# Kernel tuning notes

Hardware: AMD Instinct MI355X
Metric: run time of the kernel (lower is better)

Reference implementation:

```python
import jax, jax.numpy as jnp
import numpy as np

B, L, D, K, V = 128, 50, 64, 1024, 100000


def setup_inputs() -> dict:
    key = jax.random.key(0)
    ks = jax.random.split(key, 10)
    s = 0.05
    return {
        "history_item_ids": jax.random.randint(ks[0], (B, L), 0, V, dtype=jnp.int32),
        "history_item_masks": jax.random.randint(ks[1], (B, L), 0, 2, dtype=jnp.int32),
        "embedding_table": jax.random.normal(ks[2], (V, D), jnp.float32) * s,
        "code_book": jax.random.normal(ks[3], (K, D), jnp.float32) * 0.1,
        "Wq": jax.random.normal(ks[4], (D, D), jnp.float32) * s,
        "bq": jnp.zeros((D,), jnp.float32),
        "Wk": jax.random.normal(ks[5], (D, D), jnp.float32) * s,
        "bk": jnp.zeros((D,), jnp.float32),
        "Wv": jax.random.normal(ks[6], (D, D), jnp.float32) * s,
        "bv": jnp.zeros((D,), jnp.float32),
        "W_enc": jax.random.normal(ks[7], (2 * D, D), jnp.float32) * s,
        "b_enc": jnp.zeros((D,), jnp.float32),
    }


def reference(history_item_ids, history_item_masks, embedding_table, code_book,
              Wq, bq, Wk, bk, Wv, bv, W_enc, b_enc):
    # mask out padded history positions
    mask = (history_item_masks >= 1).astype(jnp.float32)          # [B, L]
    h = embedding_table[history_item_ids] * mask[..., None]       # [B, L, D]

    # self_attn: attention over ALL B*L flattened tokens (cross-batch, as original)
    flat = h.reshape(-1, D)                                       # [B*L, D]
    q = flat @ Wq + bq
    k = flat @ Wk + bk
    v = flat @ Wv + bv
    scores = (q @ k.T) / jnp.sqrt(jnp.float32(D))                 # [B*L, B*L]
    h = (jax.nn.softmax(scores, axis=-1) @ v).reshape(B, L, D)

    denom = mask.sum(axis=1, keepdims=True)                       # [B, 1]
    hist_mean = h.sum(axis=1) / (denom + 1e-9)                    # [B, D]

    # get_quantized: pairwise sq distances + argmin + codebook lookup
    f = h.reshape(-1, D)                                          # [B*L, D]
    d2 = (jnp.sum(f * f, axis=1, keepdims=True)
          + jnp.sum(code_book * code_book, axis=1)
          - 2.0 * f @ code_book.T)                                # [B*L, K]
    idx = jnp.argmin(d2, axis=1)                                  # [B*L]
    vq = code_book[idx].reshape(B, L, D)                          # one_hot @ code_book == gather
    vq_mean = vq.sum(axis=1) / denom                              # [B, D]

    x = jnp.concatenate([vq_mean, hist_mean], axis=-1)            # [B, 2D]
    return x @ W_enc + b_enc                                      # [B, D]
```

## Files before the change

### kernel.cpp

```cpp
#include <hip/hip_runtime.h>

typedef __attribute__((ext_vector_type(8))) short bf16x8_t;
typedef __attribute__((ext_vector_type(4))) float f32x4_t;

#define B_   128
#define L_   50
#define D_   64
#define N_   6400
#define KC   1024
#define STRD 72

static __device__ __forceinline__ unsigned short f2b(float x) {
    union { float f; unsigned int u; } c; c.f = x;
    return (unsigned short)((c.u + 0x7FFFu + ((c.u >> 16) & 1u)) >> 16);
}

__global__ __launch_bounds__(256) void k_qkv(
    const int* __restrict__ ids, const int* __restrict__ masks,
    const float* __restrict__ emb,
    const float* __restrict__ Wq, const float* __restrict__ bq,
    const float* __restrict__ Wk, const float* __restrict__ bk,
    const float* __restrict__ Wv, const float* __restrict__ bv,
    const float* __restrict__ cbf, const float* __restrict__ benc,
    unsigned short* __restrict__ q, unsigned short* __restrict__ k,
    unsigned short* __restrict__ vt,
    float* __restrict__ cn, unsigned short* __restrict__ cbb,
    float* __restrict__ out)
{
    const int tid = threadIdx.x;
    if (blockIdx.x >= 404) {
        for (int i = tid; i < B_ * 64; i += 256) out[i] = benc[i & 63];
        return;
    }
    if (blockIdx.x >= 400) {
        const int c = (blockIdx.x - 400) * 256 + tid;
        float s = 0.f;
        #pragma unroll
        for (int d4 = 0; d4 < 16; ++d4) {
            float4 x = ((const float4*)cbf)[c * 16 + d4];
            s = fmaf(x.x, x.x, s); s = fmaf(x.y, x.y, s);
            s = fmaf(x.z, x.z, s); s = fmaf(x.w, x.w, s);
            ushort4 u;
            u.x = f2b(x.x); u.y = f2b(x.y); u.z = f2b(x.z); u.w = f2b(x.w);
            *(ushort4*)&cbb[c * 64 + d4 * 4] = u;
        }
        cn[c] = s;
        return;
    }

    __shared__ float Ws[3 * 64 * 64];
    __shared__ float hs[16][64];
    const int n0  = blockIdx.x * 16;

    {
        const float4* wq4 = (const float4*)Wq;
        const float4* wk4 = (const float4*)Wk;
        const float4* wv4 = (const float4*)Wv;
        float4* ws4 = (float4*)Ws;
        #pragma unroll
        for (int i = 0; i < 4; ++i) ws4[i*256 + tid]        = wq4[i*256 + tid];
        #pragma unroll
        for (int i = 0; i < 4; ++i) ws4[1024 + i*256 + tid] = wk4[i*256 + tid];
        #pragma unroll
        for (int i = 0; i < 4; ++i) ws4[2048 + i*256 + tid] = wv4[i*256 + tid];
    }
    {
        const int t  = tid >> 4, c4 = tid & 15;
        const int n  = n0 + t;
        const int id = ids[n];
        const float m = (masks[n] >= 1) ? 1.0f : 0.0f;
        float4 e = ((const float4*)emb)[id * 16 + c4];
        ((float4*)&hs[t][0])[c4] = make_float4(e.x*m, e.y*m, e.z*m, e.w*m);
    }
    __syncthreads();

    const int j  = tid & 63;
    const int tg = tid >> 6;
    const float bqj = bq[j], bkj = bk[j], bvj = bv[j];
    #pragma unroll
    for (int p = 0; p < 4; ++p) {
        const int t = p * 4 + tg;
        float aq = bqj, ak = bkj, av = bvj;
        #pragma unroll 8
        for (int d = 0; d < 64; ++d) {
            const float hd = hs[t][d];
            aq = fmaf(hd, Ws[d*64 + j],        aq);
            ak = fmaf(hd, Ws[4096 + d*64 + j], ak);
            av = fmaf(hd, Ws[8192 + d*64 + j], av);
        }
        const int n = n0 + t;
        q[n*64 + j]   = f2b(aq);
        k[n*64 + j]   = f2b(ak);
        vt[j*N_ + n]  = f2b(av);
    }
}

__global__ __launch_bounds__(256, 4) void k_attn(
    const unsigned short* __restrict__ qg, const unsigned short* __restrict__ kg,
    const unsigned short* __restrict__ vtg,
    float* __restrict__ opart, float* __restrict__ lpart)
{
    __shared__ unsigned short Qs[32 * STRD];
    __shared__ unsigned short Ks[64 * STRD];
    __shared__ unsigned short Vts[64 * STRD];
    __shared__ unsigned short Ps[32 * STRD];
    __shared__ float Of[32 * 66];
    __shared__ float lred[2][32];

    const int tid  = threadIdx.x;
    const int qt   = blockIdx.x >> 2;
    const int sp   = blockIdx.x & 3;
    const int q0   = qt * 32;
    const int kvb  = sp * 1600;
    const int lane = tid & 63;
    const int w    = tid >> 6;
    const int m    = w & 1;
    const int s    = w >> 1;
    const int lr   = lane & 15;
    const int lg   = lane >> 4;

    {
        const int row = tid >> 3, ch = tid & 7;
        uint4 t = *(const uint4*)&qg[(q0 + row) * 64 + ch * 8];
        *(uint4*)&Qs[row * STRD + ch * 8] = t;
    }
    __syncthreads();
    const bf16x8_t qa0 = *(const bf16x8_t*)&Qs[(m*16 + lr) * STRD +  0 + lg*8];
    const bf16x8_t qa1 = *(const bf16x8_t*)&Qs[(m*16 + lr) * STRD + 32 + lg*8];

    f32x4_t o0 = {0.f,0.f,0.f,0.f}, o1 = {0.f,0.f,0.f,0.f};
    f32x4_t o2 = {0.f,0.f,0.f,0.f}, o3 = {0.f,0.f,0.f,0.f};
    float ls0 = 0.f, ls1 = 0.f, ls2 = 0.f, ls3 = 0.f;
    const float scale = 0.125f;

    for (int st = 0; st < 25; ++st) {
        __syncthreads();
        const int j0 = kvb + st * 64;
        {
            const int row = tid >> 3, ch = tid & 7;
            uint4 a = *(const uint4*)&kg [(j0 + row)      * 64 + ch*8];
            uint4 b = *(const uint4*)&kg [(j0 + row + 32) * 64 + ch*8];
            uint4 c = *(const uint4*)&vtg[ row       * N_ + j0 + ch*8];
            uint4 d = *(const uint4*)&vtg[(row + 32) * N_ + j0 + ch*8];
            *(uint4*)&Ks [ row      * STRD + ch*8] = a;
            *(uint4*)&Ks [(row+32)  * STRD + ch*8] = b;
            *(uint4*)&Vts[ row      * STRD + ch*8] = c;
            *(uint4*)&Vts[(row+32)  * STRD + ch*8] = d;
        }
        __syncthreads();

        #pragma unroll
        for (int t = 0; t < 2; ++t) {
            const int kcol = s*32 + t*16 + lr;
            bf16x8_t kb0 = *(const bf16x8_t*)&Ks[kcol * STRD +  0 + lg*8];
            bf16x8_t kb1 = *(const bf16x8_t*)&Ks[kcol * STRD + 32 + lg*8];
            f32x4_t acc = {0.f,0.f,0.f,0.f};
            acc = __builtin_amdgcn_mfma_f32_16x16x32_bf16(qa0, kb0, acc, 0, 0, 0);
            acc = __builtin_amdgcn_mfma_f32_16x16x32_bf16(qa1, kb1, acc, 0, 0, 0);
            const float p0 = __expf(acc[0] * scale);
            const float p1 = __expf(acc[1] * scale);
            const float p2 = __expf(acc[2] * scale);
            const float p3 = __expf(acc[3] * scale);
            ls0 += p0; ls1 += p1; ls2 += p2; ls3 += p3;
            const int rb = (m*16 + lg*4) * STRD + kcol;
            Ps[rb           ] = f2b(p0);
            Ps[rb +   STRD  ] = f2b(p1);
            Ps[rb + 2*STRD  ] = f2b(p2);
            Ps[rb + 3*STRD  ] = f2b(p3);
        }

        const bf16x8_t pa = *(const bf16x8_t*)&Ps[(m*16 + lr) * STRD + s*32 + lg*8];
        {
            bf16x8_t vb;
            vb = *(const bf16x8_t*)&Vts[( 0 + lr) * STRD + s*32 + lg*8];
            o0 = __builtin_amdgcn_mfma_f32_16x16x32_bf16(pa, vb, o0, 0, 0, 0);
            vb = *(const bf16x8_t*)&Vts[(16 + lr) * STRD + s*32 + lg*8];
            o1 = __builtin_amdgcn_mfma_f32_16x16x32_bf16(pa, vb, o1, 0, 0, 0);
            vb = *(const bf16x8_t*)&Vts[(32 + lr) * STRD + s*32 + lg*8];
            o2 = __builtin_amdgcn_mfma_f32_16x16x32_bf16(pa, vb, o2, 0, 0, 0);
            vb = *(const bf16x8_t*)&Vts[(48 + lr) * STRD + s*32 + lg*8];
            o3 = __builtin_amdgcn_mfma_f32_16x16x32_bf16(pa, vb, o3, 0, 0, 0);
        }
    }

    #pragma unroll
    for (int off = 1; off <= 8; off <<= 1) {
        ls0 += __shfl_xor(ls0, off);
        ls1 += __shfl_xor(ls1, off);
        ls2 += __shfl_xor(ls2, off);
        ls3 += __shfl_xor(ls3, off);
    }
    if (lr == 0) {
        const int rb = m*16 + lg*4;
        lred[s][rb    ] = ls0;
        lred[s][rb + 1] = ls1;
        lred[s][rb + 2] = ls2;
        lred[s][rb + 3] = ls3;
    }

    if (s == 0) {
        #pragma unroll
        for (int r = 0; r < 4; ++r) {
            const int row = m*16 + lg*4 + r;
            Of[row*66 +  0 + lr] = o0[r];
            Of[row*66 + 16 + lr] = o1[r];
            Of[row*66 + 32 + lr] = o2[r];
            Of[row*66 + 48 + lr] = o3[r];
        }
    }
    __syncthreads();
    if (s == 1) {
        float* op = opart + ((size_t)sp * N_ + q0) * 64;
        #pragma unroll
        for (int r = 0; r < 4; ++r) {
            const int row = m*16 + lg*4 + r;
            op[row*64 +  0 + lr] = Of[row*66 +  0 + lr] + o0[r];
            op[row*64 + 16 + lr] = Of[row*66 + 16 + lr] + o1[r];
            op[row*64 + 32 + lr] = Of[row*66 + 32 + lr] + o2[r];
            op[row*64 + 48 + lr] = Of[row*66 + 48 + lr] + o3[r];
        }
    }
    if (tid < 32) lpart[sp*N_ + q0 + tid] = lred[0][tid] + lred[1][tid];
}

__global__ __launch_bounds__(64) void k_vq(
    const float* __restrict__ opart, const float* __restrict__ lpart,
    const unsigned short* __restrict__ cbb, const float* __restrict__ cn,
    const float* __restrict__ cbf, const int* __restrict__ masks,
    const float* __restrict__ Wenc, float* __restrict__ out)
{
    const int lane = threadIdx.x;
    const int n0   = blockIdx.x * 16;
    const int lr   = lane & 15, lg = lane >> 4;
    const int row  = n0 + lr;

    const float l = lpart[row] + lpart[N_ + row] + lpart[2*N_ + row] + lpart[3*N_ + row];
    const float inv = 1.0f / l;

    float fr[16];
    #pragma unroll
    for (int h = 0; h < 2; ++h) {
        const int base = row*64 + h*32 + lg*8;
        float4 s0 = *(const float4*)&opart[base];
        float4 s1 = *(const float4*)&opart[(size_t)N_*64   + base];
        float4 s2 = *(const float4*)&opart[(size_t)N_*64*2 + base];
        float4 s3 = *(const float4*)&opart[(size_t)N_*64*3 + base];
        float4 t0 = *(const float4*)&opart[base + 4];
        float4 t1 = *(const float4*)&opart[(size_t)N_*64   + base + 4];
        float4 t2 = *(const float4*)&opart[(size_t)N_*64*2 + base + 4];
        float4 t3 = *(const float4*)&opart[(size_t)N_*64*3 + base + 4];
        fr[h*8+0] = ((s0.x+s1.x)+s2.x)+s3.x;  fr[h*8+1] = ((s0.y+s1.y)+s2.y)+s3.y;
        fr[h*8+2] = ((s0.z+s1.z)+s2.z)+s3.z;  fr[h*8+3] = ((s0.w+s1.w)+s2.w)+s3.w;
        fr[h*8+4] = ((t0.x+t1.x)+t2.x)+t3.x;  fr[h*8+5] = ((t0.y+t1.y)+t2.y)+t3.y;
        fr[h*8+6] = ((t0.z+t1.z)+t2.z)+t3.z;  fr[h*8+7] = ((t0.w+t1.w)+t2.w)+t3.w;
    }
    bf16x8_t fa0, fa1;
    #pragma unroll
    for (int i = 0; i < 8; ++i) {
        fa0[i] = (short)f2b(fr[i]     * inv);
        fa1[i] = (short)f2b(fr[8 + i] * inv);
    }

    float best0 = 3.0e38f, best1 = 3.0e38f, best2 = 3.0e38f, best3 = 3.0e38f;
    int   bi0 = 0, bi1 = 0, bi2 = 0, bi3 = 0;

    #pragma unroll 4
    for (int st = 0; st < 64; ++st) {
        const int crow = st * 16 + lr;
        bf16x8_t cb0 = *(const bf16x8_t*)&cbb[crow * 64 +  0 + lg*8];
        bf16x8_t cb1 = *(const bf16x8_t*)&cbb[crow * 64 + 32 + lg*8];
        const float cnv = cn[crow];
        f32x4_t acc = {0.f,0.f,0.f,0.f};
        acc = __builtin_amdgcn_mfma_f32_16x16x32_bf16(fa0, cb0, acc, 0, 0, 0);
        acc = __builtin_amdgcn_mfma_f32_16x16x32_bf16(fa1, cb1, acc, 0, 0, 0);
        const float d0 = fmaf(-2.f, acc[0], cnv);
        const float d1 = fmaf(-2.f, acc[1], cnv);
        const float d2 = fmaf(-2.f, acc[2], cnv);
        const float d3 = fmaf(-2.f, acc[3], cnv);
        if (d0 < best0) { best0 = d0; bi0 = crow; }
        if (d1 < best1) { best1 = d1; bi1 = crow; }
        if (d2 < best2) { best2 = d2; bi2 = crow; }
        if (d3 < best3) { best3 = d3; bi3 = crow; }
    }

    #pragma unroll
    for (int off = 1; off <= 8; off <<= 1) {
        float ov; int oi;
        ov = __shfl_xor(best0, off); oi = __shfl_xor(bi0, off);
        if (ov < best0 || (ov == best0 && oi < bi0)) { best0 = ov; bi0 = oi; }
        ov = __shfl_xor(best1, off); oi = __shfl_xor(bi1, off);
        if (ov < best1 || (ov == best1 && oi < bi1)) { best1 = ov; bi1 = oi; }
        ov = __shfl_xor(best2, off); oi = __shfl_xor(bi2, off);
        if (ov < best2 || (ov == best2 && oi < bi2)) { best2 = ov; bi2 = oi; }
        ov = __shfl_xor(best3, off); oi = __shfl_xor(bi3, off);
        if (ov < best3 || (ov == best3 && oi < bi3)) { best3 = ov; bi3 = oi; }
    }

    const int d  = lane;
    const int b0 = n0 / 50;
    const int r0 = n0 - b0 * 50;
    float vq0 = 0.f, hi0 = 0.f, vq1 = 0.f, hi1 = 0.f;
    #pragma unroll
    for (int t = 0; t < 16; ++t) {
        int ci;
        switch (t & 3) {
            case 0:  ci = __shfl(bi0, (t >> 2) * 16); break;
            case 1:  ci = __shfl(bi1, (t >> 2) * 16); break;
            case 2:  ci = __shfl(bi2, (t >> 2) * 16); break;
            default: ci = __shfl(bi3, (t >> 2) * 16); break;
        }
        const float invt = __shfl(inv, t);
        const int   nb   = (n0 + t) * 64 + d;
        const float hv = (((opart[nb] + opart[(size_t)N_*64 + nb])
                         + opart[(size_t)N_*64*2 + nb]) + opart[(size_t)N_*64*3 + nb]) * invt;
        const float vv = cbf[ci * 64 + d];
        if (r0 + t < 50) { vq0 += vv; hi0 += hv; }
        else             { vq1 += vv; hi1 += hv; }
    }

    int mv0 = (lane < 50) ? ((masks[b0*50 + lane] >= 1) ? 1 : 0) : 0;
    #pragma unroll
    for (int off = 1; off <= 32; off <<= 1) mv0 += __shfl_xor(mv0, off);
    const float dn0 = (float)mv0;

    {
        const float iv = 1.0f / dn0, ih = 1.0f / (dn0 + 1e-9f);
        float c0 = 0.f;
        #pragma unroll 8
        for (int dp = 0; dp < 64; ++dp) {
            c0 = fmaf(__shfl(vq0, dp) * iv, Wenc[dp*64 + d], c0);
            c0 = fmaf(__shfl(hi0, dp) * ih, Wenc[(64 + dp)*64 + d], c0);
        }
        atomicAdd(&out[b0*64 + d], c0);
    }
    if (r0 + 15 >= 50) {
        const int b1 = b0 + 1;
        int mv1 = (lane < 50) ? ((masks[b1*50 + lane] >= 1) ? 1 : 0) : 0;
        #pragma unroll
        for (int off = 1; off <= 32; off <<= 1) mv1 += __shfl_xor(mv1, off);
        const float dn1 = (float)mv1;
        const float iv = 1.0f / dn1, ih = 1.0f / (dn1 + 1e-9f);
        float c1 = 0.f;
        #pragma unroll 8
        for (int dp = 0; dp < 64; ++dp) {
            c1 = fmaf(__shfl(vq1, dp) * iv, Wenc[dp*64 + d], c1);
            c1 = fmaf(__shfl(hi1, dp) * ih, Wenc[(64 + dp)*64 + d], c1);
        }
        atomicAdd(&out[b1*64 + d], c1);
    }
}

extern "C" void kernel_launch(void* const* d_in, const int* in_sizes, int n_in,
                              void* d_out, int out_size, void* d_ws, size_t ws_size,
                              hipStream_t stream)
{
    const int*   ids   = (const int*)  d_in[0];
    const int*   masks = (const int*)  d_in[1];
    const float* emb   = (const float*)d_in[2];
    const float* cb    = (const float*)d_in[3];
    const float* Wq    = (const float*)d_in[4];
    const float* bq    = (const float*)d_in[5];
    const float* Wk    = (const float*)d_in[6];
    const float* bk    = (const float*)d_in[7];
    const float* Wv    = (const float*)d_in[8];
    const float* bv    = (const float*)d_in[9];
    const float* Wenc  = (const float*)d_in[10];
    const float* benc  = (const float*)d_in[11];
    float* out = (float*)d_out;

    char* w = (char*)d_ws;
    unsigned short* qb    = (unsigned short*)(w);
    unsigned short* kb    = (unsigned short*)(w +  819200);
    unsigned short* vtb   = (unsigned short*)(w + 1638400);
    float*          opart = (float*)        (w + 2457600);
    float*          lpart = (float*)        (w + 9011200);
    float*          cn    = (float*)        (w + 9113600);
    unsigned short* cbb   = (unsigned short*)(w + 9117696);

    hipLaunchKernelGGL(k_qkv,  dim3(405), dim3(256), 0, stream,
                       ids, masks, emb, Wq, bq, Wk, bk, Wv, bv, cb, benc,
                       qb, kb, vtb, cn, cbb, out);
    hipLaunchKernelGGL(k_attn, dim3(800), dim3(256), 0, stream,
                       qb, kb, vtb, opart, lpart);
    hipLaunchKernelGGL(k_vq,   dim3(400), dim3(64),  0, stream,
                       opart, lpart, cbb, cn, cb, masks, Wenc, out);
}
```

Before: 157.7 us.

## Fuse VQ epilogue into attention kernel via last-split-block counter

Removes the separate k_vq launch by having the last of the four KV-split blocks of each query tile, detected with an atomic counter after a threadfence, run the split merge, codebook argmin and encoder projection. Two waves of that block each handle 16 rows, in place of the former 64-thread blocks. The counters are zeroed in the first kernel. This saves one kernel launch and its tail gap, at the cost of serialising the epilogue behind the slowest split and adding fences and atomics to every attention block.

```diff
diff --git a/kernel.cpp b/kernel.cpp
--- a/kernel.cpp
+++ b/kernel.cpp
@@ -25,11 +25,12 @@
     unsigned short* __restrict__ q, unsigned short* __restrict__ k,
     unsigned short* __restrict__ vt,
     float* __restrict__ cn, unsigned short* __restrict__ cbb,
-    float* __restrict__ out)
+    float* __restrict__ out, unsigned int* __restrict__ cnt)
 {
     const int tid = threadIdx.x;
     if (blockIdx.x >= 404) {
         for (int i = tid; i < B_ * 64; i += 256) out[i] = benc[i & 63];
+        if (tid < 200) cnt[tid] = 0u;
         return;
     }
     if (blockIdx.x >= 400) {
@@ -98,7 +99,11 @@
 __global__ __launch_bounds__(256, 4) void k_attn(
     const unsigned short* __restrict__ qg, const unsigned short* __restrict__ kg,
     const unsigned short* __restrict__ vtg,
-    float* __restrict__ opart, float* __restrict__ lpart)
+    float* __restrict__ opart, float* __restrict__ lpart,
+    const unsigned short* __restrict__ cbb, const float* __restrict__ cn,
+    const float* __restrict__ cbf, const int* __restrict__ masks,
+    const float* __restrict__ Wenc, float* __restrict__ out,
+    unsigned int* __restrict__ cnt)
 {
     __shared__ unsigned short Qs[32 * STRD];
     __shared__ unsigned short Ks[64 * STRD];
@@ -106,6 +111,7 @@
     __shared__ unsigned short Ps[32 * STRD];
     __shared__ float Of[32 * 66];
     __shared__ float lred[2][32];
+    __shared__ int lastFlag;
 
     const int tid  = threadIdx.x;
     const int qt   = blockIdx.x >> 2;
@@ -221,132 +227,135 @@
         }
     }
     if (tid < 32) lpart[sp*N_ + q0 + tid] = lred[0][tid] + lred[1][tid];
-}
-
-__global__ __launch_bounds__(64) void k_vq(
-    const float* __restrict__ opart, const float* __restrict__ lpart,
-    const unsigned short* __restrict__ cbb, const float* __restrict__ cn,
-    const float* __restrict__ cbf, const int* __restrict__ masks,
-    const float* __restrict__ Wenc, float* __restrict__ out)
-{
-    const int lane = threadIdx.x;
-    const int n0   = blockIdx.x * 16;
-    const int lr   = lane & 15, lg = lane >> 4;
-    const int row  = n0 + lr;
-
-    const float l = lpart[row] + lpart[N_ + row] + lpart[2*N_ + row] + lpart[3*N_ + row];
-    const float inv = 1.0f / l;
-
-    float fr[16];
-    #pragma unroll
-    for (int h = 0; h < 2; ++h) {
-        const int base = row*64 + h*32 + lg*8;
-        float4 s0 = *(const float4*)&opart[base];
-        float4 s1 = *(const float4*)&opart[(size_t)N_*64   + base];
-        float4 s2 = *(const float4*)&opart[(size_t)N_*64*2 + base];
-        float4 s3 = *(const float4*)&opart[(size_t)N_*64*3 + base];
-        float4 t0 = *(const float4*)&opart[base + 4];
-        float4 t1 = *(const float4*)&opart[(size_t)N_*64   + base + 4];
-        float4 t2 = *(const float4*)&opart[(size_t)N_*64*2 + base + 4];
-        float4 t3 = *(const float4*)&opart[(size_t)N_*64*3 + base + 4];
-        fr[h*8+0] = ((s0.x+s1.x)+s2.x)+s3.x;  fr[h*8+1] = ((s0.y+s1.y)+s2.y)+s3.y;
-        fr[h*8+2] = ((s0.z+s1.z)+s2.z)+s3.z;  fr[h*8+3] = ((s0.w+s1.w)+s2.w)+s3.w;
-        fr[h*8+4] = ((t0.x+t1.x)+t2.x)+t3.x;  fr[h*8+5] = ((t0.y+t1.y)+t2.y)+t3.y;
-        fr[h*8+6] = ((t0.z+t1.z)+t2.z)+t3.z;  fr[h*8+7] = ((t0.w+t1.w)+t2.w)+t3.w;
-    }
-    bf16x8_t fa0, fa1;
-    #pragma unroll
-    for (int i = 0; i < 8; ++i) {
-        fa0[i] = (short)f2b(fr[i]     * inv);
-        fa1[i] = (short)f2b(fr[8 + i] * inv);
-    }
-
-    float best0 = 3.0e38f, best1 = 3.0e38f, best2 = 3.0e38f, best3 = 3.0e38f;
-    int   bi0 = 0, bi1 = 0, bi2 = 0, bi3 = 0;
-
-    #pragma unroll 4
-    for (int st = 0; st < 64; ++st) {
-        const int crow = st * 16 + lr;
-        bf16x8_t cb0 = *(const bf16x8_t*)&cbb[crow * 64 +  0 + lg*8];
-        bf16x8_t cb1 = *(const bf16x8_t*)&cbb[crow * 64 + 32 + lg*8];
-        const float cnv = cn[crow];
-        f32x4_t acc = {0.f,0.f,0.f,0.f};
-        acc = __builtin_amdgcn_mfma_f32_16x16x32_bf16(fa0, cb0, acc, 0, 0, 0);
-        acc = __builtin_amdgcn_mfma_f32_16x16x32_bf16(fa1, cb1, acc, 0, 0, 0);
-        const float d0 = fmaf(-2.f, acc[0], cnv);
-        const float d1 = fmaf(-2.f, acc[1], cnv);
-        const float d2 = fmaf(-2.f, acc[2], cnv);
-        const float d3 = fmaf(-2.f, acc[3], cnv);
-        if (d0 < best0) { best0 = d0; bi0 = crow; }
-        if (d1 < best1) { best1 = d1; bi1 = crow; }
-        if (d2 < best2) { best2 = d2; bi2 = crow; }
-        if (d3 < best3) { best3 = d3; bi3 = crow; }
-    }
-
-    #pragma unroll
-    for (int off = 1; off <= 8; off <<= 1) {
-        float ov; int oi;
-        ov = __shfl_xor(best0, off); oi = __shfl_xor(bi0, off);
-        if (ov < best0 || (ov == best0 && oi < bi0)) { best0 = ov; bi0 = oi; }
-        ov = __shfl_xor(best1, off); oi = __shfl_xor(bi1, off);
-        if (ov < best1 || (ov == best1 && oi < bi1)) { best1 = ov; bi1 = oi; }
-        ov = __shfl_xor(best2, off); oi = __shfl_xor(bi2, off);
-        if (ov < best2 || (ov == best2 && oi < bi2)) { best2 = ov; bi2 = oi; }
-        ov = __shfl_xor(best3, off); oi = __shfl_xor(bi3, off);
-        if (ov < best3 || (ov == best3 && oi < bi3)) { best3 = ov; bi3 = oi; }
-    }
-
-    const int d  = lane;
-    const int b0 = n0 / 50;
-    const int r0 = n0 - b0 * 50;
-    float vq0 = 0.f, hi0 = 0.f, vq1 = 0.f, hi1 = 0.f;
-    #pragma unroll
-    for (int t = 0; t < 16; ++t) {
-        int ci;
-        switch (t & 3) {
-            case 0:  ci = __shfl(bi0, (t >> 2) * 16); break;
-            case 1:  ci = __shfl(bi1, (t >> 2) * 16); break;
-            case 2:  ci = __shfl(bi2, (t >> 2) * 16); break;
-            default: ci = __shfl(bi3, (t >> 2) * 16); break;
-        }
-        const float invt = __shfl(inv, t);
-        const int   nb   = (n0 + t) * 64 + d;
-        const float hv = (((opart[nb] + opart[(size_t)N_*64 + nb])
-                         + opart[(size_t)N_*64*2 + nb]) + opart[(size_t)N_*64*3 + nb]) * invt;
-        const float vv = cbf[ci * 64 + d];
-        if (r0 + t < 50) { vq0 += vv; hi0 += hv; }
-        else             { vq1 += vv; hi1 += hv; }
-    }
-
-    int mv0 = (lane < 50) ? ((masks[b0*50 + lane] >= 1) ? 1 : 0) : 0;
-    #pragma unroll
-    for (int off = 1; off <= 32; off <<= 1) mv0 += __shfl_xor(mv0, off);
-    const float dn0 = (float)mv0;
-
+
+    __threadfence();
+    __syncthreads();
+    if (tid == 0) lastFlag = (atomicAdd(&cnt[qt], 1u) == 3u);
+    __syncthreads();
+    if (!lastFlag) return;
+    __threadfence();
+
+    if (tid >= 128) return;
     {
-        const float iv = 1.0f / dn0, ih = 1.0f / (dn0 + 1e-9f);
-        float c0 = 0.f;
-        #pragma unroll 8
-        for (int dp = 0; dp < 64; ++dp) {
-            c0 = fmaf(__shfl(vq0, dp) * iv, Wenc[dp*64 + d], c0);
-            c0 = fmaf(__shfl(hi0, dp) * ih, Wenc[(64 + dp)*64 + d], c0);
-        }
-        atomicAdd(&out[b0*64 + d], c0);
-    }
-    if (r0 + 15 >= 50) {
-        const int b1 = b0 + 1;
-        int mv1 = (lane < 50) ? ((masks[b1*50 + lane] >= 1) ? 1 : 0) : 0;
-        #pragma unroll
-        for (int off = 1; off <= 32; off <<= 1) mv1 += __shfl_xor(mv1, off);
-        const float dn1 = (float)mv1;
-        const float iv = 1.0f / dn1, ih = 1.0f / (dn1 + 1e-9f);
-        float c1 = 0.f;
-        #pragma unroll 8
-        for (int dp = 0; dp < 64; ++dp) {
-            c1 = fmaf(__shfl(vq1, dp) * iv, Wenc[dp*64 + d], c1);
-            c1 = fmaf(__shfl(hi1, dp) * ih, Wenc[(64 + dp)*64 + d], c1);
-        }
-        atomicAdd(&out[b1*64 + d], c1);
+        const int n0  = q0 + w * 16;
+        const int row = n0 + lr;
+
+        const float l = lpart[row] + lpart[N_ + row]
+                      + lpart[2*N_ + row] + lpart[3*N_ + row];
+        const float inv = 1.0f / l;
+
+        float fr[16];
+        #pragma unroll
+        for (int h = 0; h < 2; ++h) {
+            const int base = row*64 + h*32 + lg*8;
+            float4 s0 = *(const float4*)&opart[base];
+            float4 s1 = *(const float4*)&opart[(size_t)N_*64   + base];
+            float4 s2 = *(const float4*)&opart[(size_t)N_*64*2 + base];
+            float4 s3 = *(const float4*)&opart[(size_t)N_*64*3 + base];
+            float4 t0 = *(const float4*)&opart[base + 4];
+            float4 t1 = *(const float4*)&opart[(size_t)N_*64   + base + 4];
+            float4 t2 = *(const float4*)&opart[(size_t)N_*64*2 + base + 4];
+            float4 t3 = *(const float4*)&opart[(size_t)N_*64*3 + base + 4];
+            fr[h*8+0] = ((s0.x+s1.x)+s2.x)+s3.x;  fr[h*8+1] = ((s0.y+s1.y)+s2.y)+s3.y;
+            fr[h*8+2] = ((s0.z+s1.z)+s2.z)+s3.z;  fr[h*8+3] = ((s0.w+s1.w)+s2.w)+s3.w;
+            fr[h*8+4] = ((t0.x+t1.x)+t2.x)+t3.x;  fr[h*8+5] = ((t0.y+t1.y)+t2.y)+t3.y;
+            fr[h*8+6] = ((t0.z+t1.z)+t2.z)+t3.z;  fr[h*8+7] = ((t0.w+t1.w)+t2.w)+t3.w;
+        }
+        bf16x8_t fa0, fa1;
+        #pragma unroll
+        for (int i = 0; i < 8; ++i) {
+            fa0[i] = (short)f2b(fr[i]     * inv);
+            fa1[i] = (short)f2b(fr[8 + i] * inv);
+        }
+
+        float best0 = 3.0e38f, best1 = 3.0e38f, best2 = 3.0e38f, best3 = 3.0e38f;
+        int   bi0 = 0, bi1 = 0, bi2 = 0, bi3 = 0;
+
+        #pragma unroll 4
+        for (int st = 0; st < 64; ++st) {
+            const int crow = st * 16 + lr;
+            bf16x8_t cb0 = *(const bf16x8_t*)&cbb[crow * 64 +  0 + lg*8];
+            bf16x8_t cb1 = *(const bf16x8_t*)&cbb[crow * 64 + 32 + lg*8];
+            const float cnv = cn[crow];
+            f32x4_t acc = {0.f,0.f,0.f,0.f};
+            acc = __builtin_amdgcn_mfma_f32_16x16x32_bf16(fa0, cb0, acc, 0, 0, 0);
+            acc = __builtin_amdgcn_mfma_f32_16x16x32_bf16(fa1, cb1, acc, 0, 0, 0);
+            const float d0 = fmaf(-2.f, acc[0], cnv);
+            const float d1 = fmaf(-2.f, acc[1], cnv);
+            const float d2 = fmaf(-2.f, acc[2], cnv);
+            const float d3 = fmaf(-2.f, acc[3], cnv);
+            if (d0 < best0) { best0 = d0; bi0 = crow; }
+            if (d1 < best1) { best1 = d1; bi1 = crow; }
+            if (d2 < best2) { best2 = d2; bi2 = crow; }
+            if (d3 < best3) { best3 = d3; bi3 = crow; }
+        }
+
+        #pragma unroll
+        for (int off = 1; off <= 8; off <<= 1) {
+            float ov; int oi;
+            ov = __shfl_xor(best0, off); oi = __shfl_xor(bi0, off);
+            if (ov < best0 || (ov == best0 && oi < bi0)) { best0 = ov; bi0 = oi; }
+            ov = __shfl_xor(best1, off); oi = __shfl_xor(bi1, off);
+            if (ov < best1 || (ov == best1 && oi < bi1)) { best1 = ov; bi1 = oi; }
+            ov = __shfl_xor(best2, off); oi = __shfl_xor(bi2, off);
+            if (ov < best2 || (ov == best2 && oi < bi2)) { best2 = ov; bi2 = oi; }
+            ov = __shfl_xor(best3, off); oi = __shfl_xor(bi3, off);
+            if (ov < best3 || (ov == best3 && oi < bi3)) { best3 = ov; bi3 = oi; }
+        }
+
+        const int d  = lane;
+        const int b0 = n0 / 50;
+        const int r0 = n0 - b0 * 50;
+        float vq0 = 0.f, hi0 = 0.f, vq1 = 0.f, hi1 = 0.f;
+        #pragma unroll
+        for (int t = 0; t < 16; ++t) {
+            int ci;
+            switch (t & 3) {
+                case 0:  ci = __shfl(bi0, (t >> 2) * 16); break;
+                case 1:  ci = __shfl(bi1, (t >> 2) * 16); break;
+                case 2:  ci = __shfl(bi2, (t >> 2) * 16); break;
+                default: ci = __shfl(bi3, (t >> 2) * 16); break;
+            }
+            const float invt = __shfl(inv, t);
+            const int   nb   = (n0 + t) * 64 + d;
+            const float hv = (((opart[nb] + opart[(size_t)N_*64 + nb])
+                             + opart[(size_t)N_*64*2 + nb])
+                             + opart[(size_t)N_*64*3 + nb]) * invt;
+            const float vv = cbf[ci * 64 + d];
+            if (r0 + t < 50) { vq0 += vv; hi0 += hv; }
+            else             { vq1 += vv; hi1 += hv; }
+        }
+
+        int mv0 = (lane < 50) ? ((masks[b0*50 + lane] >= 1) ? 1 : 0) : 0;
+        #pragma unroll
+        for (int off = 1; off <= 32; off <<= 1) mv0 += __shfl_xor(mv0, off);
+        const float dn0 = (float)mv0;
+
+        {
+            const float iv = 1.0f / dn0, ih = 1.0f / (dn0 + 1e-9f);
+            float c0 = 0.f;
+            #pragma unroll 8
+            for (int dp = 0; dp < 64; ++dp) {
+                c0 = fmaf(__shfl(vq0, dp) * iv, Wenc[dp*64 + d], c0);
+                c0 = fmaf(__shfl(hi0, dp) * ih, Wenc[(64 + dp)*64 + d], c0);
+            }
+            atomicAdd(&out[b0*64 + d], c0);
+        }
+        if (r0 + 15 >= 50) {
+            const int b1 = b0 + 1;
+            int mv1 = (lane < 50) ? ((masks[b1*50 + lane] >= 1) ? 1 : 0) : 0;
+            #pragma unroll
+            for (int off = 1; off <= 32; off <<= 1) mv1 += __shfl_xor(mv1, off);
+            const float dn1 = (float)mv1;
+            const float iv = 1.0f / dn1, ih = 1.0f / (dn1 + 1e-9f);
+            float c1 = 0.f;
+            #pragma unroll 8
+            for (int dp = 0; dp < 64; ++dp) {
+                c1 = fmaf(__shfl(vq1, dp) * iv, Wenc[dp*64 + d], c1);
+                c1 = fmaf(__shfl(hi1, dp) * ih, Wenc[(64 + dp)*64 + d], c1);
+            }
+            atomicAdd(&out[b1*64 + d], c1);
+        }
     }
 }
 
@@ -376,12 +385,12 @@
     float*          lpart = (float*)        (w + 9011200);
     float*          cn    = (float*)        (w + 9113600);
     unsigned short* cbb   = (unsigned short*)(w + 9117696);
+    unsigned int*   cnt   = (unsigned int*) (w + 9248768);
 
     hipLaunchKernelGGL(k_qkv,  dim3(405), dim3(256), 0, stream,
                        ids, masks, emb, Wq, bq, Wk, bk, Wv, bv, cb, benc,
-                       qb, kb, vtb, cn, cbb, out);
+                       qb, kb, vtb, cn, cbb, out, cnt);
     hipLaunchKernelGGL(k_attn, dim3(800), dim3(256), 0, stream,
-                       qb, kb, vtb, opart, lpart);
-    hipLaunchKernelGGL(k_vq,   dim3(400), dim3(64),  0, stream,
-                       opart, lpart, cbb, cn, cb, masks, Wenc, out);
+                       qb, kb, vtb, opart, lpart, cbb, cn, cb, masks,
+                       Wenc, out, cnt);
 }
```

Measured after the change: 316.9 us. 2.01x slower.
